# Kernel optimization log

Hardware: AMD Instinct MI355X
Metric: run time of the kernel (lower is better)

## Reference

```python
import jax, jax.numpy as jnp
import numpy as np

OUT_C, IN_C, KS, KN = 256, 256, 3, 4
TEMP = 1.0
D1 = OUT_C * KS            # 768
D2 = IN_C * KS             # 768
D2R = D2 // 2 + 1          # 385 (rfft width)


def _freq_indices():
    # mirror torch get_fft2freq(d1, d2, use_rfft=True)
    fh = np.fft.fftfreq(D1)
    fw = np.fft.rfftfreq(D2)
    grid = np.stack(np.meshgrid(fh, fw, indexing='ij'), axis=-1)  # (D1, D2R, 2)
    dist = np.linalg.norm(grid, axis=-1).ravel()
    idx = np.argsort(dist, kind='stable')
    return (idx // D2R).astype(np.int32), (idx % D2R).astype(np.int32)


def setup_inputs() -> dict:
    key = jax.random.key(0)
    k1, k2, k3 = jax.random.split(key, 3)
    b, h, w = 8, 64, 64
    fh, fw = _freq_indices()
    num_freq = fh.shape[0]  # 295680 = D1 * D2R (param_reduction == 1.0)
    return {
        'x': jax.random.normal(k1, (b, IN_C, h, w), dtype=jnp.float32),
        'dft_weight': jax.random.normal(k2, (KN, num_freq, 2), dtype=jnp.float32) * 1e-6,
        'k_att': jax.random.normal(k3, (b, KN, 1, 1), dtype=jnp.float32),
        'freq_h': jnp.asarray(fh),
        'freq_w': jnp.asarray(fw),
    }


def reference(x, dft_weight, k_att, freq_h, freq_w):
    b, c, h, w = x.shape
    # kernel attention: sigmoid(att / temp) * 2 / kernel_num
    att = jax.nn.sigmoid(k_att / TEMP) * (2.0 / KN)          # (b, KN, 1, 1)
    # weighted sum of per-kernel frequency weights -> (b, F, 2)
    wsum = jnp.einsum('knf,bk->bnf', dft_weight, att.reshape(b, KN))
    wc = jax.lax.complex(wsum[..., 0], wsum[..., 1])          # (b, F) complex
    # scatter into dense rfft2 map (indices are a permutation: no duplicates)
    dft_map = jnp.zeros((b, D1, D2R), dtype=jnp.complex64)
    dft_map = dft_map.at[:, freq_h, freq_w].set(wc)
    # inverse rFFT2 -> spatial weights (b, D1, D2)
    sw = jnp.fft.irfft2(dft_map, s=(D1, D2))
    # (b, out, ks, in, ks) -> (b, out, in, ks, ks) -> grouped-conv kernel
    wk = sw.reshape(b, OUT_C, KS, IN_C, KS).transpose(0, 1, 3, 2, 4)
    wk = wk.reshape(b * OUT_C, IN_C, KS, KS)
    # batch of per-sample convs == one grouped conv with groups=b
    xg = x.reshape(1, b * c, h, w)
    out = jax.lax.conv_general_dilated(
        xg, wk, window_strides=(1, 1), padding=[(1, 1), (1, 1)],
        dimension_numbers=('NCHW', 'OIHW', 'NCHW'), feature_group_count=b)
    return out.reshape(b, OUT_C, out.shape[2], out.shape[3])
```

## Files before the change

kernel.cpp:

```cpp
#include <hip/hip_runtime.h>
#include <math.h>

#define D1 768
#define D2R 385
#define NF 295680
#define KNUM 4
#define NB 8
#define NC 256
#define TWOPI_768 0.008181230868723419f
#define INV768 0.0013020833333333333f

#define ATW_U32 1572864u
#define YA_U32 2752512u
#define T_U32 3981312u
#define SPECB_K_U32 344064u
#define WBF_BYTE 9437184u

typedef __attribute__((ext_vector_type(8))) short short8;
typedef __attribute__((ext_vector_type(16))) float f32x16;
union U4S8 { unsigned int u[4]; uint4 u4; short8 s8; };

static __device__ __forceinline__ unsigned int f2bf(float f) {
  unsigned int u = __float_as_uint(f);
  return (u + 0x7fffu + ((u >> 16) & 1u)) >> 16;
}

static __device__ __forceinline__ void sincos_rev768(int idx, float* s,
                                                     float* c) {
  float rev = (float)idx * INV768;
  *s = __builtin_amdgcn_sinf(rev);
  *c = __builtin_amdgcn_cosf(rev);
}

static __device__ __forceinline__ void barrier_lgkm() {
  asm volatile("s_waitcnt lgkmcnt(0)" ::: "memory");
  __builtin_amdgcn_sched_barrier(0);
  __builtin_amdgcn_s_barrier();
  __builtin_amdgcn_sched_barrier(0);
}

__global__ __launch_bounds__(256) void prep_kernel(
    const float* __restrict__ dw, const int* __restrict__ fh,
    const int* __restrict__ fw, unsigned int* __restrict__ ws) {
  int q = blockIdx.x * 256 + threadIdx.x;
  if (q < 295680) {
    int k = q / 73920;
    int ql = q - k * 73920;
    long f2i = (long)k * NF + (long)ql * 4;
    const float4 v0 = ((const float4*)dw)[f2i >> 1];
    const float4 v1 = ((const float4*)dw)[(f2i >> 1) + 1];
    const int4 h4 = ((const int4*)fh)[ql];
    const int4 c4 = ((const int4*)fw)[ql];
    size_t kb = (size_t)k * SPECB_K_U32;
    ws[kb + (size_t)c4.x * 768 + h4.x] = f2bf(v0.x) | (f2bf(v0.y) << 16);
    ws[kb + (size_t)c4.y * 768 + h4.y] = f2bf(v0.z) | (f2bf(v0.w) << 16);
    ws[kb + (size_t)c4.z * 768 + h4.z] = f2bf(v1.x) | (f2bf(v1.y) << 16);
    ws[kb + (size_t)c4.w * 768 + h4.w] = f2bf(v1.z) | (f2bf(v1.w) << 16);
    return;
  }
  int j = q - 295680;
  if (j < 294912) {
    int j0 = j * 4;
    int ri = j0 / 589824;
    int rem = j0 - ri * 589824;
    int m = rem / 768, h0 = rem - (rem / 768) * 768;
    uint4 o;
#pragma unroll
    for (int e = 0; e < 4; ++e) {
      int idx = ((h0 + e) * m) % 768;
      float s, c;
      sincos_rev768(idx, &s, &c);
      unsigned lo, hi;
      if (ri == 0) { lo = f2bf(c); hi = f2bf(-s); }
      else         { lo = f2bf(s); hi = f2bf(c); }
      ((unsigned*)&o)[e] = lo | (hi << 16);
    }
    *(uint4*)(ws + ATW_U32 + j0) = o;
  } else if (j < 371712) {
    int p0 = (j - 294912) * 4;
    int n = p0 / 400, cc0 = p0 - (p0 / 400) * 400;
    uint4 o;
#pragma unroll
    for (int e = 0; e < 4; ++e) {
      int cc = cc0 + e;
      unsigned v = 0;
      if (cc <= 384) {
        float wgt = (cc == 0 || cc == 384) ? 1.6954210069444445e-6f
                                           : 3.390842013888889e-6f;
        int idx = (cc * n) % 768;
        float s, c;
        sincos_rev768(idx, &s, &c);
        v = f2bf(wgt * c) | (f2bf(-wgt * s) << 16);
      }
      ((unsigned*)&o)[e] = v;
    }
    *(uint4*)(ws + T_U32 + (size_t)n * 400 + cc0) = o;
  } else if (j < 420096) {
    int p0 = (j - 371712) * 4;
    int k = p0 / 48384;
    int r = p0 - k * 48384;
    int row = 385 + r / 768;
    int col = r - (r / 768) * 768;
    *(uint4*)(ws + (size_t)k * SPECB_K_U32 + (size_t)row * 768 + col) =
        make_uint4(0u, 0u, 0u, 0u);
  } else if (j < 431616) {
    int p0 = (j - 420096) * 4;
#pragma unroll
    for (int e = 0; e < 4; ++e) {
      int p = p0 + e;
      int k = p / 11520;
      int r = p - k * 11520;
      int m = r / 15, jj = r - (r / 15) * 15;
      ws[YA_U32 + (size_t)k * 307200 + (size_t)m * 400 + 385 + jj] = 0u;
    }
  }
}

__global__ __launch_bounds__(256) void fftA_kernel(
    const unsigned short* __restrict__ Atw,
    const unsigned short* __restrict__ specB,
    unsigned short* __restrict__ Ya) {
  __shared__ __align__(16) unsigned short Al[2][64 * 40], Bl[2][64 * 40];
  int t = threadIdx.x;
  int mt = blockIdx.x, nt = blockIdx.y, z = blockIdx.z;
  int ri = z & 1, k = z >> 1;
  const unsigned short* Ag =
      Atw + (size_t)ri * 1179648 + (size_t)(mt * 64) * 1536;
  const unsigned short* Bg =
      specB + (size_t)k * 688128 + (size_t)(nt * 64) * 1536;
  int rowS = t >> 2, q = t & 3;
  int lane = t & 63, w = t >> 6;
  int mq = w & 1, nq = w >> 1;
  int lm = lane & 31, half = lane >> 5;
  int wr = rowS * 40 + q * 8;
  int ao = (mq * 32 + lm) * 40 + half * 8;
  int bo = (nq * 32 + lm) * 40 + half * 8;

  f32x16 acc;
#pragma unroll
  for (int r = 0; r < 16; ++r) acc[r] = 0.f;

#define FA_LOAD(da, db, kb)                                              \
  da = *(const uint4*)(Ag + (size_t)rowS * 1536 + (kb) * 32 + q * 8);    \
  db = *(const uint4*)(Bg + (size_t)rowS * 1536 + (kb) * 32 + q * 8);
#define F_WRITE(buf, sa, sb)                                             \
  *(uint4*)&Al[buf][wr] = sa;                                            \
  *(uint4*)&Bl[buf][wr] = sb;
#define F_COMPUTE(buf)                                                   \
  {                                                                      \
    const unsigned short* Ab = Al[buf];                                  \
    const unsigned short* Bb = Bl[buf];                                  \
    _Pragma("unroll") for (int kk2 = 0; kk2 < 2; ++kk2) {                \
      short8 a8 = *(const short8*)&Ab[ao + kk2 * 16];                    \
      short8 b8 = *(const short8*)&Bb[bo + kk2 * 16];                    \
      acc = __builtin_amdgcn_mfma_f32_32x32x16_bf16(a8, b8, acc, 0, 0, 0); \
    }                                                                    \
  }

  uint4 eA, eB, oA, oB;
  FA_LOAD(eA, eB, 0)
  FA_LOAD(oA, oB, 1)
  F_WRITE(0, eA, eB)
  barrier_lgkm();

  const int NK = 48;
  for (int kb = 0; kb < NK; kb += 2) {
    if (kb + 2 < NK) { FA_LOAD(eA, eB, kb + 2) }
    F_COMPUTE(0)
    if (kb + 1 < NK) { F_WRITE(1, oA, oB) }
    barrier_lgkm();
    if (kb + 1 < NK) {
      if (kb + 3 < NK) { FA_LOAD(oA, oB, kb + 3) }
      F_COMPUTE(1)
      if (kb + 2 < NK) { F_WRITE(0, eA, eB) }
      barrier_lgkm();
    }
  }

  int c = nt * 64 + nq * 32 + lm;
  if (c < D2R) {
    unsigned short* Yk = Ya + (size_t)k * 614400;
    int mb = mt * 64 + mq * 32 + 4 * half;
#pragma unroll
    for (int reg = 0; reg < 16; ++reg) {
      int m = mb + (reg & 3) + 8 * (reg >> 2);
      Yk[(size_t)m * 800 + 2 * c + ri] = (unsigned short)f2bf(acc[reg]);
    }
  }
}

__global__ __launch_bounds__(256) void fftB_kernel(
    const unsigned short* __restrict__ Ya, const unsigned short* __restrict__ T,
    float* __restrict__ SW) {
  __shared__ __align__(16) unsigned short Al[2][64 * 40], Bl[2][64 * 40];
  int t = threadIdx.x;
  int mt = blockIdx.x, nt = blockIdx.y, k = blockIdx.z;
  const unsigned short* Ag = Ya + (size_t)k * 614400 + (size_t)(mt * 64) * 800;
  const unsigned short* Bg = T + (size_t)(nt * 64) * 800;
  int rowS = t >> 2, q = t & 3;
  int lane = t & 63, w = t >> 6;
  int mq = w & 1, nq = w >> 1;
  int lm = lane & 31, half = lane >> 5;
  int wr = rowS * 40 + q * 8;
  int ao = (mq * 32 + lm) * 40 + half * 8;
  int bo = (nq * 32 + lm) * 40 + half * 8;

  f32x16 acc;
#pragma unroll
  for (int r = 0; r < 16; ++r) acc[r] = 0.f;

#define FB_LOAD(da, db, kb)                                             \
  da = *(const uint4*)(Ag + (size_t)rowS * 800 + (kb) * 32 + q * 8);    \
  db = *(const uint4*)(Bg + (size_t)rowS * 800 + (kb) * 32 + q * 8);

  uint4 eA, eB, oA, oB;
  FB_LOAD(eA, eB, 0)
  FB_LOAD(oA, oB, 1)
  F_WRITE(0, eA, eB)
  barrier_lgkm();

  const int NK = 25;
  for (int kb = 0; kb < NK; kb += 2) {
    if (kb + 2 < NK) { FB_LOAD(eA, eB, kb + 2) }
    F_COMPUTE(0)
    if (kb + 1 < NK) { F_WRITE(1, oA, oB) }
    barrier_lgkm();
    if (kb + 1 < NK) {
      if (kb + 3 < NK) { FB_LOAD(oA, oB, kb + 3) }
      F_COMPUTE(1)
      if (kb + 2 < NK) { F_WRITE(0, eA, eB) }
      barrier_lgkm();
    }
  }

  float* SWk = SW + (size_t)k * 589824;
  int n = nt * 64 + nq * 32 + lm;
  int mb = mt * 64 + mq * 32 + 4 * half;
#pragma unroll
  for (int reg = 0; reg < 16; ++reg) {
    int m = mb + (reg & 3) + 8 * (reg >> 2);
    SWk[(size_t)m * 768 + n] = acc[reg];
  }
}

__global__ __launch_bounds__(256) void wprep_kernel(
    const float* __restrict__ ka, const float* __restrict__ SW,
    unsigned short* __restrict__ wBF) {
  __shared__ float rowL[4][768];
  int t = threadIdx.x;
  int row = blockIdx.x;
  int oc = row / 3, dy = row - oc * 3;
  if (t < 192) {
#pragma unroll
    for (int k = 0; k < 4; ++k)
      *(float4*)&rowL[k][t * 4] =
          *(const float4*)(SW + (size_t)k * 589824 + (size_t)row * 768 + t * 4);
  }
  float att[8][4];
#pragma unroll
  for (int b = 0; b < 8; ++b)
#pragma unroll
    for (int k = 0; k < 4; ++k)
      att[b][k] = 0.5f / (1.f + expf(-ka[b * 4 + k]));
  __syncthreads();
  int icb = t >> 4, i = t & 15;
#pragma unroll
  for (int dx = 0; dx < 3; ++dx) {
    int col = icb * 48 + dx + 3 * i;
    float v0 = rowL[0][col], v1 = rowL[1][col], v2 = rowL[2][col],
          v3 = rowL[3][col];
    int s = dy * 3 + dx;
#pragma unroll
    for (int b = 0; b < 8; ++b) {
      float v = att[b][0] * v0 + att[b][1] * v1 + att[b][2] * v2 +
                att[b][3] * v3;
      wBF[(((size_t)(b * 16 + icb) * 9 + s) * 256 + oc) * 16 + i] =
          (unsigned short)f2bf(v);
    }
  }
}

__global__ __launch_bounds__(256, 2) void conv_mfma_kernel(
    const float* __restrict__ x, const unsigned short* __restrict__ wBF,
    float* __restrict__ out) {
  __shared__ __align__(16) unsigned char ldsX[2][4 * 2 * 66 * 16];
  int t = threadIdx.x;
  int orig = blockIdx.x;
  int xcd = orig & 7, seq = orig >> 3;
  int slice = xcd * 2 + (seq >> 5);
  int pxt = seq & 31;
  int b = slice >> 1, oct = slice & 1;
  int py0 = pxt * 2, oc0 = oct * 128;
  int lane = t & 63, w = t >> 6;
  int ocq = w >> 1, pxq = w & 1;
  int n = lane & 31, half = lane >> 5;

  if (t < 128) {
    int buf = t >> 6, rem = t & 63;
    int idx = rem >> 2, word = rem & 3;
    int r = idx >> 2, icg = (idx >> 1) & 1, c = (idx & 1) ? 65 : 0;
    *(unsigned int*)(&ldsX[buf][(((r * 2 + icg) * 66) + c) * 16 + word * 4]) =
        0u;
  }

  f32x16 acc[2][2];
#pragma unroll
  for (int i = 0; i < 2; ++i)
#pragma unroll
    for (int j = 0; j < 2; ++j)
#pragma unroll
      for (int r = 0; r < 16; ++r) acc[i][j][r] = 0.f;

  int px4 = lane & 15, sub = lane >> 4;
  int iy = py0 - 1 + sub;
  bool valid = (iy >= 0 && iy < 64);
  const float* xpb =
      x + (((size_t)(b * NC + w * 4)) * 64 + (valid ? iy : 0)) * 64 + px4;
  int xwbase = (((sub * 2 + (w >> 1)) * 66) + 1 + px4) * 16 + (w & 1) * 8;
  unsigned char* xw0 = (unsigned char*)&ldsX[0][0] + xwbase;
  unsigned char* xw1 = (unsigned char*)&ldsX[1][0] + xwbase;

  float a[4][4];
#pragma unroll
  for (int j = 0; j < 4; ++j)
#pragma unroll
    for (int pp = 0; pp < 4; ++pp) a[j][pp] = 0.f;
  if (valid) {
#pragma unroll
    for (int j = 0; j < 4; ++j) {
      const float* pj = xpb + (size_t)j * 4096;
#pragma unroll
      for (int pp = 0; pp < 4; ++pp) a[j][pp] = pj[pp * 16];
    }
  }

  const uint4* wg4 = (const uint4*)wBF;
  size_t abase =
      (size_t)b * 144 * 512 + (size_t)(oc0 + ocq * 64 + n) * 2 + half;
  U4S8 pf[9][2];
#pragma unroll
  for (int i = 0; i < 9; ++i) {
    pf[i][0].u4 = wg4[abase + (size_t)i * 512];
    pf[i][1].u4 = wg4[abase + (size_t)i * 512 + 64];
  }

#pragma unroll
  for (int pp = 0; pp < 4; ++pp) {
    uint2 wv;
    wv.x = f2bf(a[0][pp]) | (f2bf(a[1][pp]) << 16);
    wv.y = f2bf(a[2][pp]) | (f2bf(a[3][pp]) << 16);
    *(uint2*)(xw0 + pp * 256) = wv;
  }
  barrier_lgkm();

  for (int icb = 0; icb < 16; ++icb) {
#pragma unroll
    for (int j = 0; j < 4; ++j)
#pragma unroll
      for (int pp = 0; pp < 4; ++pp) a[j][pp] = 0.f;
    if (icb < 15 && valid) {
      const float* p0 = xpb + (size_t)(icb + 1) * 16 * 4096;
#pragma unroll
      for (int j = 0; j < 4; ++j) {
        const float* pj = p0 + (size_t)j * 4096;
#pragma unroll
        for (int pp = 0; pp < 4; ++pp) a[j][pp] = pj[pp * 16];
      }
    }
    const unsigned char* bufR = &ldsX[icb & 1][0];
#pragma unroll
    for (int s = 0; s < 9; ++s) {
      int step = icb * 9 + s;
      int dy = s / 3, dx = s - dy * 3;
      const unsigned char* bb =
          bufR + ((((pxq + dy) * 2 + half) * 66) + n + dx) * 16;
      short8 B0 = *(const short8*)bb;
      short8 B1 = *(const short8*)(bb + 512);
      acc[0][0] = __builtin_amdgcn_mfma_f32_32x32x16_bf16(pf[s][0].s8, B0,
                                                          acc[0][0], 0, 0, 0);
      acc[0][1] = __builtin_amdgcn_mfma_f32_32x32x16_bf16(pf[s][0].s8, B1,
                                                          acc[0][1], 0, 0, 0);
      acc[1][0] = __builtin_amdgcn_mfma_f32_32x32x16_bf16(pf[s][1].s8, B0,
                                                          acc[1][0], 0, 0, 0);
      acc[1][1] = __builtin_amdgcn_mfma_f32_32x32x16_bf16(pf[s][1].s8, B1,
                                                          acc[1][1], 0, 0, 0);
      if (icb < 15) {
        pf[s][0].u4 = wg4[abase + (size_t)(step + 9) * 512];
        pf[s][1].u4 = wg4[abase + (size_t)(step + 9) * 512 + 64];
      }
    }
    if (icb < 15) {
      unsigned char* xw = (icb & 1) ? xw0 : xw1;
#pragma unroll
      for (int pp = 0; pp < 4; ++pp) {
        uint2 wv;
        wv.x = f2bf(a[0][pp]) | (f2bf(a[1][pp]) << 16);
        wv.y = f2bf(a[2][pp]) | (f2bf(a[3][pp]) << 16);
        *(uint2*)(xw + pp * 256) = wv;
      }
    }
    barrier_lgkm();
  }

  int py = py0 + pxq;
#pragma unroll
  for (int osub = 0; osub < 2; ++osub)
#pragma unroll
    for (int psub = 0; psub < 2; ++psub) {
      int OC = oc0 + ocq * 64 + osub * 32 + 4 * half;
      int pxc = psub * 32 + n;
      float* op = out + (((size_t)(b * NC + OC)) * 64 + py) * 64 + pxc;
#pragma unroll
      for (int reg = 0; reg < 16; ++reg) {
        int ocm = (reg & 3) + 8 * (reg >> 2);
        op[(size_t)ocm * 4096] = acc[osub][psub][reg];
      }
    }
}

extern "C" void kernel_launch(void* const* d_in, const int* in_sizes, int n_in,
                              void* d_out, int out_size, void* d_ws,
                              size_t ws_size, hipStream_t stream) {
  const float* x = (const float*)d_in[0];
  const float* dw = (const float*)d_in[1];
  const float* ka = (const float*)d_in[2];
  const int* fh = (const int*)d_in[3];
  const int* fw = (const int*)d_in[4];
  float* out = (float*)d_out;
  unsigned int* ws = (unsigned int*)d_ws;
  const unsigned short* specB = (const unsigned short*)d_ws;
  const unsigned short* Atw = (const unsigned short*)((char*)d_ws + 6291456);
  unsigned short* Ya = (unsigned short*)((char*)d_ws + 11010048);
  const unsigned short* T = (const unsigned short*)((char*)d_ws + 15925248);
  float* SW = (float*)d_ws;
  unsigned short* wBF = (unsigned short*)((char*)d_ws + WBF_BYTE);

  hipLaunchKernelGGL(prep_kernel, dim3(2841), dim3(256), 0, stream, dw, fh,
                     fw, ws);
  hipLaunchKernelGGL(fftA_kernel, dim3(12, 7, 8), dim3(256), 0, stream, Atw,
                     specB, Ya);
  hipLaunchKernelGGL(fftB_kernel, dim3(12, 12, KNUM), dim3(256), 0, stream, Ya,
                     T, SW);
  hipLaunchKernelGGL(wprep_kernel, dim3(768), dim3(256), 0, stream, ka, SW,
                     wBF);
  hipLaunchKernelGGL(conv_mfma_kernel, dim3(512), dim3(256), 0, stream, x,
                     wBF, out);
}
```

Baseline: 184.6 us.

## Stage per-block conv weights through LDS instead of per-wave register prefetch

Changes the bf16 weight layout written by the weight-build kernel so each (batch, step, half) slice is contiguous over output channels. The conv kernel then loads each icb's 9 weight slices cooperatively into a shared LDS tile and reads the MFMA A operands from LDS. Previously each wave fetched its own weights from global into a large register prefetch array. The intent is to cut duplicate global weight traffic across the two pixel waves and lower register pressure. In exchange it adds an extra barrier per icb, since the weight buffer is single-buffered, plus about 36KB more LDS, which may limit occupancy.

```diff
diff --git a/kernel.cpp b/kernel.cpp
--- a/kernel.cpp
+++ b/kernel.cpp
@@ -264,17 +264,19 @@
       att[b][k] = 0.5f / (1.f + expf(-ka[b * 4 + k]));
   __syncthreads();
   int icb = t >> 4, i = t & 15;
+  int ih = i >> 3, il = i & 7;
 #pragma unroll
   for (int dx = 0; dx < 3; ++dx) {
     int col = icb * 48 + dx + 3 * i;
     float v0 = rowL[0][col], v1 = rowL[1][col], v2 = rowL[2][col],
           v3 = rowL[3][col];
     int s = dy * 3 + dx;
+    int step = icb * 9 + s;
 #pragma unroll
     for (int b = 0; b < 8; ++b) {
       float v = att[b][0] * v0 + att[b][1] * v1 + att[b][2] * v2 +
                 att[b][3] * v3;
-      wBF[(((size_t)(b * 16 + icb) * 9 + s) * 256 + oc) * 16 + i] =
+      wBF[(((size_t)(b * 144 + step) * 2 + ih) * 256 + oc) * 8 + il] =
           (unsigned short)f2bf(v);
     }
   }
@@ -284,6 +286,7 @@
     const float* __restrict__ x, const unsigned short* __restrict__ wBF,
     float* __restrict__ out) {
   __shared__ __align__(16) unsigned char ldsX[2][4 * 2 * 66 * 16];
+  __shared__ __align__(16) unsigned char wL[9 * 2 * 128 * 16];
   int t = threadIdx.x;
   int orig = blockIdx.x;
   int xcd = orig & 7, seq = orig >> 3;
@@ -320,84 +323,76 @@
   unsigned char* xw0 = (unsigned char*)&ldsX[0][0] + xwbase;
   unsigned char* xw1 = (unsigned char*)&ldsX[1][0] + xwbase;
 
+  const unsigned short* wgB = wBF + (size_t)b * 589824 +
+                              (size_t)(t >> 7) * 2048 +
+                              (size_t)(oc0 + (t & 127)) * 8;
+  unsigned char* wlw = wL + ((t >> 7) * 128 + (t & 127)) * 16;
+  const unsigned char* wlr =
+      wL + (lane >> 5) * 2048 + (ocq * 64 + (lane & 31)) * 16;
+
+  uint4 wreg[9];
+#define WSTAGE_LOAD(ICB)                                                  \
+  _Pragma("unroll") for (int s9 = 0; s9 < 9; ++s9) wreg[s9] =             \
+      *(const uint4*)(wgB + (size_t)((ICB) * 9 + s9) * 4096);
+#define WSTAGE_WRITE()                                                    \
+  _Pragma("unroll") for (int s9 = 0; s9 < 9; ++s9)                        \
+      *(uint4*)(wlw + s9 * 4096) = wreg[s9];
+
   float a[4][4];
-#pragma unroll
-  for (int j = 0; j < 4; ++j)
-#pragma unroll
-    for (int pp = 0; pp < 4; ++pp) a[j][pp] = 0.f;
-  if (valid) {
-#pragma unroll
-    for (int j = 0; j < 4; ++j) {
-      const float* pj = xpb + (size_t)j * 4096;
-#pragma unroll
-      for (int pp = 0; pp < 4; ++pp) a[j][pp] = pj[pp * 16];
-    }
-  }
-
-  const uint4* wg4 = (const uint4*)wBF;
-  size_t abase =
-      (size_t)b * 144 * 512 + (size_t)(oc0 + ocq * 64 + n) * 2 + half;
-  U4S8 pf[9][2];
-#pragma unroll
-  for (int i = 0; i < 9; ++i) {
-    pf[i][0].u4 = wg4[abase + (size_t)i * 512];
-    pf[i][1].u4 = wg4[abase + (size_t)i * 512 + 64];
-  }
-
-#pragma unroll
-  for (int pp = 0; pp < 4; ++pp) {
-    uint2 wv;
-    wv.x = f2bf(a[0][pp]) | (f2bf(a[1][pp]) << 16);
-    wv.y = f2bf(a[2][pp]) | (f2bf(a[3][pp]) << 16);
-    *(uint2*)(xw0 + pp * 256) = wv;
-  }
+#define XLOAD(ICB)                                                        \
+  _Pragma("unroll") for (int j = 0; j < 4; ++j) _Pragma("unroll")         \
+      for (int pp = 0; pp < 4; ++pp) a[j][pp] = 0.f;                      \
+  if (valid) {                                                            \
+    const float* p0 = xpb + (size_t)(ICB) * 16 * 4096;                    \
+    _Pragma("unroll") for (int j = 0; j < 4; ++j) {                       \
+      const float* pj = p0 + (size_t)j * 4096;                            \
+      _Pragma("unroll") for (int pp = 0; pp < 4; ++pp)                    \
+          a[j][pp] = pj[pp * 16];                                         \
+    }                                                                     \
+  }
+#define XWRITE(XW)                                                        \
+  _Pragma("unroll") for (int pp = 0; pp < 4; ++pp) {                      \
+    uint2 wv;                                                             \
+    wv.x = f2bf(a[0][pp]) | (f2bf(a[1][pp]) << 16);                       \
+    wv.y = f2bf(a[2][pp]) | (f2bf(a[3][pp]) << 16);                       \
+    *(uint2*)((XW) + pp * 256) = wv;                                      \
+  }
+
+  WSTAGE_LOAD(0)
+  XLOAD(0)
+  WSTAGE_WRITE()
+  XWRITE(xw0)
   barrier_lgkm();
 
   for (int icb = 0; icb < 16; ++icb) {
-#pragma unroll
-    for (int j = 0; j < 4; ++j)
-#pragma unroll
-      for (int pp = 0; pp < 4; ++pp) a[j][pp] = 0.f;
-    if (icb < 15 && valid) {
-      const float* p0 = xpb + (size_t)(icb + 1) * 16 * 4096;
-#pragma unroll
-      for (int j = 0; j < 4; ++j) {
-        const float* pj = p0 + (size_t)j * 4096;
-#pragma unroll
-        for (int pp = 0; pp < 4; ++pp) a[j][pp] = pj[pp * 16];
-      }
+    if (icb < 15) {
+      WSTAGE_LOAD(icb + 1)
+      XLOAD(icb + 1)
     }
     const unsigned char* bufR = &ldsX[icb & 1][0];
 #pragma unroll
     for (int s = 0; s < 9; ++s) {
-      int step = icb * 9 + s;
       int dy = s / 3, dx = s - dy * 3;
       const unsigned char* bb =
           bufR + ((((pxq + dy) * 2 + half) * 66) + n + dx) * 16;
       short8 B0 = *(const short8*)bb;
       short8 B1 = *(const short8*)(bb + 512);
-      acc[0][0] = __builtin_amdgcn_mfma_f32_32x32x16_bf16(pf[s][0].s8, B0,
-                                                          acc[0][0], 0, 0, 0);
-      acc[0][1] = __builtin_amdgcn_mfma_f32_32x32x16_bf16(pf[s][0].s8, B1,
-                                                          acc[0][1], 0, 0, 0);
-      acc[1][0] = __builtin_amdgcn_mfma_f32_32x32x16_bf16(pf[s][1].s8, B0,
-                                                          acc[1][0], 0, 0, 0);
-      acc[1][1] = __builtin_amdgcn_mfma_f32_32x32x16_bf16(pf[s][1].s8, B1,
-                                                          acc[1][1], 0, 0, 0);
-      if (icb < 15) {
-        pf[s][0].u4 = wg4[abase + (size_t)(step + 9) * 512];
-        pf[s][1].u4 = wg4[abase + (size_t)(step + 9) * 512 + 64];
-      }
-    }
+      const unsigned char* wls = wlr + s * 4096;
+      short8 A0 = *(const short8*)wls;
+      short8 A1 = *(const short8*)(wls + 512);
+      acc[0][0] =
+          __builtin_amdgcn_mfma_f32_32x32x16_bf16(A0, B0, acc[0][0], 0, 0, 0);
+      acc[0][1] =
+          __builtin_amdgcn_mfma_f32_32x32x16_bf16(A0, B1, acc[0][1], 0, 0, 0);
+      acc[1][0] =
+          __builtin_amdgcn_mfma_f32_32x32x16_bf16(A1, B0, acc[1][0], 0, 0, 0);
+      acc[1][1] =
+          __builtin_amdgcn_mfma_f32_32x32x16_bf16(A1, B1, acc[1][1], 0, 0, 0);
+    }
+    barrier_lgkm();
     if (icb < 15) {
-      unsigned char* xw = (icb & 1) ? xw0 : xw1;
-#pragma unroll
-      for (int pp = 0; pp < 4; ++pp) {
-        uint2 wv;
-        wv.x = f2bf(a[0][pp]) | (f2bf(a[1][pp]) << 16);
-        wv.y = f2bf(a[2][pp]) | (f2bf(a[3][pp]) << 16);
-        *(uint2*)(xw + pp * 256) = wv;
-      }
+      WSTAGE_WRITE()
+      XWRITE((icb & 1) ? xw0 : xw1)
     }
     barrier_lgkm();
   }
```

After: 186.1 us. About the same (+0.8%).

## Fuse second FFT stage with attention-weighted kernel prep into one kernel

Applied to the files above, without the earlier changes.

The second inverse-DFT GEMM now computes all four kernel-basis outputs per block, sharing the B-tile loads across four accumulators, and applies the sigmoid attention mix and bf16 conversion in the epilogue. This removes the fp32 spatial-weight intermediate, its write and re-read, and the separate wprep launch. In exchange the grid shrinks from 576 to 144 blocks and each thread holds four 16-float accumulators. That cuts occupancy and parallelism, and the epilogue writes to wBF are scattered.

```diff
diff --git a/kernel.cpp b/kernel.cpp
--- a/kernel.cpp
+++ b/kernel.cpp
@@ -7,14 +7,12 @@
 #define KNUM 4
 #define NB 8
 #define NC 256
-#define TWOPI_768 0.008181230868723419f
 #define INV768 0.0013020833333333333f
 
 #define ATW_U32 1572864u
 #define YA_U32 2752512u
 #define T_U32 3981312u
 #define SPECB_K_U32 344064u
-#define WBF_BYTE 9437184u
 
 typedef __attribute__((ext_vector_type(8))) short short8;
 typedef __attribute__((ext_vector_type(16))) float f32x16;
@@ -189,13 +187,12 @@
   }
 }
 
-__global__ __launch_bounds__(256) void fftB_kernel(
+__global__ __launch_bounds__(256) void fftBW_kernel(
     const unsigned short* __restrict__ Ya, const unsigned short* __restrict__ T,
-    float* __restrict__ SW) {
-  __shared__ __align__(16) unsigned short Al[2][64 * 40], Bl[2][64 * 40];
+    const float* __restrict__ ka, unsigned short* __restrict__ wBF) {
+  __shared__ __align__(16) unsigned short Al[2][4][64 * 40], Bl[2][64 * 40];
   int t = threadIdx.x;
-  int mt = blockIdx.x, nt = blockIdx.y, k = blockIdx.z;
-  const unsigned short* Ag = Ya + (size_t)k * 614400 + (size_t)(mt * 64) * 800;
+  int mt = blockIdx.x, nt = blockIdx.y;
   const unsigned short* Bg = T + (size_t)(nt * 64) * 800;
   int rowS = t >> 2, q = t & 3;
   int lane = t & 63, w = t >> 6;
@@ -204,78 +201,75 @@
   int wr = rowS * 40 + q * 8;
   int ao = (mq * 32 + lm) * 40 + half * 8;
   int bo = (nq * 32 + lm) * 40 + half * 8;
-
-  f32x16 acc;
-#pragma unroll
-  for (int r = 0; r < 16; ++r) acc[r] = 0.f;
-
-#define FB_LOAD(da, db, kb)                                             \
-  da = *(const uint4*)(Ag + (size_t)rowS * 800 + (kb) * 32 + q * 8);    \
-  db = *(const uint4*)(Bg + (size_t)rowS * 800 + (kb) * 32 + q * 8);
-
-  uint4 eA, eB, oA, oB;
-  FB_LOAD(eA, eB, 0)
-  FB_LOAD(oA, oB, 1)
-  F_WRITE(0, eA, eB)
+  size_t arow = (size_t)(mt * 64 + rowS) * 800 + q * 8;
+
+  f32x16 acc[4];
+#pragma unroll
+  for (int k = 0; k < 4; ++k)
+#pragma unroll
+    for (int r = 0; r < 16; ++r) acc[k][r] = 0.f;
+
+  uint4 eA[4], oA[4], eB, oB;
+#define BW_LOAD(dA, dB, kb)                                                \
+  _Pragma("unroll") for (int k = 0; k < 4; ++k) dA[k] =                    \
+      *(const uint4*)(Ya + (size_t)k * 614400 + arow + (kb) * 32);         \
+  dB = *(const uint4*)(Bg + (size_t)rowS * 800 + (kb) * 32 + q * 8);
+#define BW_WRITE(buf, sA, sB)                                              \
+  _Pragma("unroll") for (int k = 0; k < 4; ++k) *(uint4*)&Al[buf][k][wr] = \
+      sA[k];                                                               \
+  *(uint4*)&Bl[buf][wr] = sB;
+#define BW_COMPUTE(buf)                                                    \
+  _Pragma("unroll") for (int kk2 = 0; kk2 < 2; ++kk2) {                    \
+    short8 b8 = *(const short8*)&Bl[buf][bo + kk2 * 16];                   \
+    _Pragma("unroll") for (int k = 0; k < 4; ++k) {                        \
+      short8 a8 = *(const short8*)&Al[buf][k][ao + kk2 * 16];              \
+      acc[k] =                                                             \
+          __builtin_amdgcn_mfma_f32_32x32x16_bf16(a8, b8, acc[k], 0, 0, 0); \
+    }                                                                      \
+  }
+
+  BW_LOAD(eA, eB, 0)
+  BW_LOAD(oA, oB, 1)
+  BW_WRITE(0, eA, eB)
   barrier_lgkm();
 
   const int NK = 25;
   for (int kb = 0; kb < NK; kb += 2) {
-    if (kb + 2 < NK) { FB_LOAD(eA, eB, kb + 2) }
-    F_COMPUTE(0)
-    if (kb + 1 < NK) { F_WRITE(1, oA, oB) }
+    if (kb + 2 < NK) { BW_LOAD(eA, eB, kb + 2) }
+    BW_COMPUTE(0)
+    if (kb + 1 < NK) { BW_WRITE(1, oA, oB) }
     barrier_lgkm();
     if (kb + 1 < NK) {
-      if (kb + 3 < NK) { FB_LOAD(oA, oB, kb + 3) }
-      F_COMPUTE(1)
-      if (kb + 2 < NK) { F_WRITE(0, eA, eB) }
+      if (kb + 3 < NK) { BW_LOAD(oA, oB, kb + 3) }
+      BW_COMPUTE(1)
+      if (kb + 2 < NK) { BW_WRITE(0, eA, eB) }
       barrier_lgkm();
     }
   }
 
-  float* SWk = SW + (size_t)k * 589824;
+  float att[8][4];
+#pragma unroll
+  for (int b = 0; b < 8; ++b)
+#pragma unroll
+    for (int k = 0; k < 4; ++k)
+      att[b][k] = 0.5f / (1.f + expf(-ka[b * 4 + k]));
   int n = nt * 64 + nq * 32 + lm;
+  int ic = n / 3, dx = n - ic * 3;
+  int icb = ic >> 4, ii = ic & 15;
   int mb = mt * 64 + mq * 32 + 4 * half;
 #pragma unroll
   for (int reg = 0; reg < 16; ++reg) {
     int m = mb + (reg & 3) + 8 * (reg >> 2);
-    SWk[(size_t)m * 768 + n] = acc[reg];
-  }
-}
-
-__global__ __launch_bounds__(256) void wprep_kernel(
-    const float* __restrict__ ka, const float* __restrict__ SW,
-    unsigned short* __restrict__ wBF) {
-  __shared__ float rowL[4][768];
-  int t = threadIdx.x;
-  int row = blockIdx.x;
-  int oc = row / 3, dy = row - oc * 3;
-  if (t < 192) {
-#pragma unroll
-    for (int k = 0; k < 4; ++k)
-      *(float4*)&rowL[k][t * 4] =
-          *(const float4*)(SW + (size_t)k * 589824 + (size_t)row * 768 + t * 4);
-  }
-  float att[8][4];
-#pragma unroll
-  for (int b = 0; b < 8; ++b)
-#pragma unroll
-    for (int k = 0; k < 4; ++k)
-      att[b][k] = 0.5f / (1.f + expf(-ka[b * 4 + k]));
-  __syncthreads();
-  int icb = t >> 4, i = t & 15;
-#pragma unroll
-  for (int dx = 0; dx < 3; ++dx) {
-    int col = icb * 48 + dx + 3 * i;
-    float v0 = rowL[0][col], v1 = rowL[1][col], v2 = rowL[2][col],
-          v3 = rowL[3][col];
+    int oc = m / 3, dy = m - oc * 3;
     int s = dy * 3 + dx;
+    size_t base = (((size_t)(icb * 9 + s)) * 256 + oc) * 16 + ii;
+    float a0 = acc[0][reg], a1 = acc[1][reg], a2 = acc[2][reg],
+          a3 = acc[3][reg];
 #pragma unroll
     for (int b = 0; b < 8; ++b) {
-      float v = att[b][0] * v0 + att[b][1] * v1 + att[b][2] * v2 +
-                att[b][3] * v3;
-      wBF[(((size_t)(b * 16 + icb) * 9 + s) * 256 + oc) * 16 + i] =
-          (unsigned short)f2bf(v);
+      float v = att[b][0] * a0 + att[b][1] * a1 + att[b][2] * a2 +
+                att[b][3] * a3;
+      wBF[base + (size_t)b * 589824] = (unsigned short)f2bf(v);
     }
   }
 }
@@ -432,17 +426,14 @@
   const unsigned short* Atw = (const unsigned short*)((char*)d_ws + 6291456);
   unsigned short* Ya = (unsigned short*)((char*)d_ws + 11010048);
   const unsigned short* T = (const unsigned short*)((char*)d_ws + 15925248);
-  float* SW = (float*)d_ws;
-  unsigned short* wBF = (unsigned short*)((char*)d_ws + WBF_BYTE);
+  unsigned short* wBF = (unsigned short*)d_ws;
 
   hipLaunchKernelGGL(prep_kernel, dim3(2841), dim3(256), 0, stream, dw, fh,
                      fw, ws);
   hipLaunchKernelGGL(fftA_kernel, dim3(12, 7, 8), dim3(256), 0, stream, Atw,
                      specB, Ya);
-  hipLaunchKernelGGL(fftB_kernel, dim3(12, 12, KNUM), dim3(256), 0, stream, Ya,
-                     T, SW);
-  hipLaunchKernelGGL(wprep_kernel, dim3(768), dim3(256), 0, stream, ka, SW,
-                     wBF);
+  hipLaunchKernelGGL(fftBW_kernel, dim3(12, 12), dim3(256), 0, stream, Ya, T,
+                     ka, wBF);
   hipLaunchKernelGGL(conv_mfma_kernel, dim3(512), dim3(256), 0, stream, x,
                      wBF, out);
 }
```

Result: slower. 213.1 us (+15.4%).
